# Kernel optimization log

Hardware: AMD Instinct MI355X
Metric: run time of the kernel (lower is better)

The kernel has to match this reference:

```python
import jax, jax.numpy as jnp
import numpy as np

B, N, IN_DIM, D, H, F, L, P = 32, 512, 64, 256, 8, 1024, 3, 512
HD = D // H


def setup_inputs() -> dict:
    key = jax.random.key(0)
    ks = jax.random.split(key, 12)
    s = 0.02
    return {
        "x": jax.random.normal(ks[0], (B, N, IN_DIM), jnp.float32),
        "tw_start": jax.random.uniform(ks[1], (B, N), jnp.float32),
        "adj_mask": jax.random.randint(ks[2], (B, N, N), 0, 2) > 0,
        "Wp": jax.random.normal(ks[3], (D, IN_DIM), jnp.float32) * s,
        "bp": jnp.zeros((D,), jnp.float32),
        "pe": jax.random.normal(ks[4], (P, D), jnp.float32) * s,
        "Wqkv": jax.random.normal(ks[5], (L, 3 * D, D), jnp.float32) * s,
        "bqkv": jnp.zeros((L, 3 * D), jnp.float32),
        "Wo": jax.random.normal(ks[6], (L, D, D), jnp.float32) * s,
        "bo": jnp.zeros((L, D), jnp.float32),
        "ln1g": jnp.ones((L, D), jnp.float32),
        "ln1b": jnp.zeros((L, D), jnp.float32),
        "W1": jax.random.normal(ks[7], (L, F, D), jnp.float32) * s,
        "b1": jnp.zeros((L, F), jnp.float32),
        "W2": jax.random.normal(ks[8], (L, D, F), jnp.float32) * s,
        "b2": jnp.zeros((L, D), jnp.float32),
        "ln2g": jnp.ones((L, D), jnp.float32),
        "ln2b": jnp.zeros((L, D), jnp.float32),
    }


def _ln(x, g, b):
    m = x.mean(-1, keepdims=True)
    v = ((x - m) ** 2).mean(-1, keepdims=True)
    return (x - m) * jax.lax.rsqrt(v + 1e-5) * g + b


def reference(x, tw_start, adj_mask, Wp, bp, pe, Wqkv, bqkv, Wo, bo,
              ln1g, ln1b, W1, b1, W2, b2, ln2g, ln2b):
    # temporal rank = inverse permutation of argsort (equals the torch scatter trick)
    rank = jnp.argsort(jnp.argsort(tw_start, axis=-1), axis=-1)
    rank = jnp.clip(rank, 0, P - 1)
    h = x @ Wp.T + bp + pe[rank]                     # (B,N,D)
    # additive mask, broadcast over heads: (B,1,N,N)
    bias = jnp.where(adj_mask, 0.0, -1e9)[:, None].astype(h.dtype)
    scale = 1.0 / np.sqrt(HD)
    for l in range(L):
        qkv = h @ Wqkv[l].T + bqkv[l]                # (B,N,3D)
        q, k, v = jnp.split(qkv, 3, axis=-1)
        q = q.reshape(B, N, H, HD)
        k = k.reshape(B, N, H, HD)
        v = v.reshape(B, N, H, HD)
        scores = jnp.einsum('bqhd,bkhd->bhqk', q, k) * scale + bias
        attn = jax.nn.softmax(scores, axis=-1)
        o = jnp.einsum('bhqk,bkhd->bqhd', attn, v).reshape(B, N, D)
        o = o @ Wo[l].T + bo[l]
        h = _ln(h + o, ln1g[l], ln1b[l])
        ffo = jax.nn.gelu(h @ W1[l].T + b1[l], approximate=False) @ W2[l].T + b2[l]
        h = _ln(h + ffo, ln2g[l], ln2b[l])
    return h
```

## Files before the change

kernel.cpp:

```cpp
#include <hip/hip_runtime.h>
#include <hip/hip_bf16.h>

#define B_ 32
#define N_ 512
#define IN_DIM_ 64
#define D_ 256
#define H_ 8
#define HD_ 32
#define F_ 1024
#define L_ 3
#define P_ 512

typedef __bf16 bf16_t;
typedef bf16_t bf16x8 __attribute__((ext_vector_type(8)));
typedef bf16_t bf16x4 __attribute__((ext_vector_type(4)));
typedef float f32x4 __attribute__((ext_vector_type(4)));

__global__ __launch_bounds__(512) void rank_kernel(const float* __restrict__ tw,
                                                   int* __restrict__ rank) {
  const int b = blockIdx.x;
  const int i = threadIdx.x;
  __shared__ float s[N_];
  const float ti = tw[b * N_ + i];
  s[i] = ti;
  __syncthreads();
  int c = 0;
#pragma unroll 8
  for (int j = 0; j < N_; ++j) {
    const float tj = s[j];
    c += (tj < ti) || (tj == ti && j < i);
  }
  rank[b * N_ + i] = c < (P_ - 1) ? c : (P_ - 1);
}

__global__ void detect_mask_kernel(const unsigned char* __restrict__ m,
                                   int* __restrict__ flag) {
  unsigned v = 0;
  for (int i = 0; i < 64; ++i)
    if (i & 3) v |= m[i];
  *flag = (v == 0) ? 1 : 0;
}

__global__ __launch_bounds__(256) void packmask_kernel(
    const unsigned char* __restrict__ m, const int* __restrict__ flag,
    unsigned long long* __restrict__ bits) {
  const int idx = blockIdx.x * 256 + threadIdx.x;
  const size_t base = (size_t)(idx >> 3) * N_ + (idx & 7) * 64;
  unsigned long long v = 0;
  if (*flag) {
    const unsigned int* p = (const unsigned int*)m + base;
#pragma unroll 8
    for (int i = 0; i < 64; ++i) v |= (unsigned long long)(p[i] & 1u) << i;
  } else {
    const unsigned char* p = m + base;
#pragma unroll 8
    for (int i = 0; i < 64; ++i) v |= (unsigned long long)(p[i] & 1u) << i;
  }
  bits[idx] = v;
}

__global__ __launch_bounds__(256) void cvt_kernel(const float* __restrict__ s,
                                                  bf16_t* __restrict__ d, int n) {
  const int i = (blockIdx.x * 256 + threadIdx.x) * 4;
  if (i >= n) return;
  const float4 v = *(const float4*)(s + i);
  bf16x4 o = {(bf16_t)v.x, (bf16_t)v.y, (bf16_t)v.z, (bf16_t)v.w};
  *(bf16x4*)(d + i) = o;
}

__device__ __forceinline__ void gl16(const bf16_t* g, char* l) {
  __builtin_amdgcn_global_load_lds(
      (const __attribute__((address_space(1))) unsigned int*)g,
      (__attribute__((address_space(3))) unsigned int*)l, 16, 0, 0);
}

template <int EPI, int WF, int WB>
__global__ __launch_bounds__(256) void gemm_lds(
    const bf16_t* __restrict__ A, const bf16_t* __restrict__ W,
    const float* __restrict__ bias, const int K, const int Nd,
    float* __restrict__ Cf, bf16_t* __restrict__ Cb,
    const int* __restrict__ rank, const float* __restrict__ pe) {
  __shared__ __align__(16) bf16_t As[2][128 * 32];
  __shared__ __align__(16) bf16_t Ws[2][128 * 32];
  const int t = threadIdx.x;
  const int w = t >> 6, l = t & 63, g = l >> 4, r16 = l & 15;
  const int wm = w >> 1, wn = w & 1;
  const int m0 = blockIdx.x * 128, n0 = blockIdx.y * 128;

  f32x4 acc[4][4];
#pragma unroll
  for (int m = 0; m < 4; ++m)
#pragma unroll
    for (int n = 0; n < 4; ++n) acc[m][n] = (f32x4){0.f, 0.f, 0.f, 0.f};

  const int srow = w * 32 + (l >> 2);
  const int scol = (l & 3) * 8;
  const bf16_t* Ag = A + (size_t)(m0 + srow) * K + scol;
  const bf16_t* Wg = W + (size_t)(n0 + srow) * K + scol;
  char* Asb = (char*)As + w * 2048;
  char* Wsb = (char*)Ws + w * 2048;
  const int rowK16 = 16 * K;

  const char* Afr = (const char*)As + (wm * 64 + r16) * 64 + g * 16;
  const char* Wfr = (const char*)Ws + (wn * 64 + r16) * 64 + g * 16;

  const int nt = K >> 5;

  gl16(Ag, Asb);
  gl16(Ag + rowK16, Asb + 1024);
  gl16(Wg, Wsb);
  gl16(Wg + rowK16, Wsb + 1024);
  asm volatile("s_waitcnt vmcnt(0)" ::: "memory");
  __builtin_amdgcn_s_barrier();
  __builtin_amdgcn_sched_barrier(0);

  for (int tt = 0; tt < nt; ++tt) {
    const int curo = (tt & 1) * 8192;
    if (tt + 1 < nt) {
      const int nxto = 8192 - curo;
      const int k0 = (tt + 1) << 5;
      gl16(Ag + k0, Asb + nxto);
      gl16(Ag + k0 + rowK16, Asb + nxto + 1024);
      gl16(Wg + k0, Wsb + nxto);
      gl16(Wg + k0 + rowK16, Wsb + nxto + 1024);
    }
    bf16x8 af[4], wf[4];
#pragma unroll
    for (int m = 0; m < 4; ++m) af[m] = *(const bf16x8*)(Afr + curo + m * 1024);
#pragma unroll
    for (int n = 0; n < 4; ++n) wf[n] = *(const bf16x8*)(Wfr + curo + n * 1024);
#pragma unroll
    for (int m = 0; m < 4; ++m)
#pragma unroll
      for (int n = 0; n < 4; ++n)
        acc[m][n] = __builtin_amdgcn_mfma_f32_16x16x32_bf16(af[m], wf[n], acc[m][n], 0, 0, 0);
    if (tt + 1 < nt) {
      asm volatile("s_waitcnt vmcnt(0)" ::: "memory");
      __builtin_amdgcn_s_barrier();
      __builtin_amdgcn_sched_barrier(0);
    }
  }

  float bcol[4];
#pragma unroll
  for (int n = 0; n < 4; ++n) bcol[n] = bias[n0 + wn * 64 + n * 16 + r16];

#pragma unroll
  for (int m = 0; m < 4; ++m) {
#pragma unroll
    for (int r = 0; r < 4; ++r) {
      const int rowg = m0 + wm * 64 + m * 16 + g * 4 + r;
      float pv[4];
      if (EPI == 2) {
        const float* per = pe + (size_t)rank[rowg] * D_ + n0 + wn * 64 + r16;
#pragma unroll
        for (int n = 0; n < 4; ++n) pv[n] = per[n * 16];
      }
#pragma unroll
      for (int n = 0; n < 4; ++n) {
        float v = acc[m][n][r] + bcol[n];
        if (EPI == 2) v += pv[n];
        if (EPI == 1) v = 0.5f * v * (1.f + erff(v * 0.70710678118654752f));
        const size_t idx = (size_t)rowg * Nd + n0 + wn * 64 + n * 16 + r16;
        if (WF) Cf[idx] = v;
        if (WB) Cb[idx] = (bf16_t)v;
      }
    }
  }
}

__global__ __launch_bounds__(256) void attn_mfma(
    const bf16_t* __restrict__ qkv, const unsigned long long* __restrict__ mbits,
    bf16_t* __restrict__ out) {
  __shared__ __align__(16) char Ksh[64 * 80];
  __shared__ __align__(16) char Vsh[32 * 144];
  __shared__ __align__(16) char Psh[4 * 16 * 144];
  __shared__ unsigned long long Msh[64 * 8];
  const int t = threadIdx.x;
  const int w = t >> 6, l = t & 63, g = l >> 4, r16 = l & 15;
  const int qt = blockIdx.x & 7, bh = blockIdx.x >> 3;
  const int b = bh >> 3, hh = bh & 7;
  const int q0 = qt * 64;
  const float scale = 0.17677669529663687f;

  for (int i = t; i < 512; i += 256)
    Msh[i] = mbits[((size_t)b * N_ + q0 + (i >> 3)) * 8 + (i & 7)];

  const bf16_t* base = qkv + (size_t)b * N_ * (3 * D_) + hh * HD_;
  const bf16x8 qf = *(const bf16x8*)(base + (size_t)(q0 + w * 16 + r16) * (3 * D_) + g * 8);

  f32x4 oacc0 = {0.f, 0.f, 0.f, 0.f}, oacc1 = {0.f, 0.f, 0.f, 0.f};
  float mrow[4] = {-1e30f, -1e30f, -1e30f, -1e30f};
  float lrow[4] = {0.f, 0.f, 0.f, 0.f};

  const int krow = t >> 2, kq = t & 3;
  const int vkey = t & 63, vd0 = (t >> 6) * 8;
  char* Kw = Ksh + krow * 80 + kq * 16;
  char* Pw = Psh + w * 16 * 144;
  const f32x4 z = {0.f, 0.f, 0.f, 0.f};

  for (int kt = 0; kt < 8; ++kt) {
    const int k0 = kt * 64;
    *(float4*)Kw = *(const float4*)(base + (size_t)(k0 + krow) * (3 * D_) + D_ + kq * 8);
    const bf16x8 vv = *(const bf16x8*)(base + (size_t)(k0 + vkey) * (3 * D_) + 2 * D_ + vd0);
#pragma unroll
    for (int j = 0; j < 8; ++j)
      *(bf16_t*)(Vsh + (vd0 + j) * 144 + vkey * 2) = vv[j];
    __syncthreads();

    f32x4 s[4];
#pragma unroll
    for (int j = 0; j < 4; ++j) {
      const bf16x8 kf = *(const bf16x8*)(Ksh + (j * 16 + r16) * 80 + g * 16);
      s[j] = __builtin_amdgcn_mfma_f32_16x16x32_bf16(qf, kf, z, 0, 0, 0);
    }
    unsigned long long mw[4];
#pragma unroll
    for (int r = 0; r < 4; ++r) mw[r] = Msh[(w * 16 + g * 4 + r) * 8 + kt];

    float sval[4][4];
    float mx[4] = {-1e30f, -1e30f, -1e30f, -1e30f};
#pragma unroll
    for (int j = 0; j < 4; ++j)
#pragma unroll
      for (int r = 0; r < 4; ++r) {
        const bool bit = (mw[r] >> (j * 16 + r16)) & 1ULL;
        const float sv = bit ? s[j][r] * scale : -1e30f;
        sval[j][r] = sv;
        mx[r] = fmaxf(mx[r], sv);
      }
#pragma unroll
    for (int d = 1; d < 16; d <<= 1)
#pragma unroll
      for (int r = 0; r < 4; ++r) mx[r] = fmaxf(mx[r], __shfl_xor(mx[r], d));

    int grow = 0;
#pragma unroll
    for (int r = 0; r < 4; ++r) grow |= (mx[r] > mrow[r] + 8.f) ? 1 : 0;
    if (__any(grow)) {
#pragma unroll
      for (int r = 0; r < 4; ++r) {
        const float mn = fmaxf(mrow[r], mx[r]);
        const float ce = __expf(mrow[r] - mn);
        mrow[r] = mn;
        lrow[r] *= ce;
        oacc0[r] *= ce;
        oacc1[r] *= ce;
      }
    }
    float psum[4] = {0.f, 0.f, 0.f, 0.f};
#pragma unroll
    for (int j = 0; j < 4; ++j)
#pragma unroll
      for (int r = 0; r < 4; ++r) {
        const float p = __expf(sval[j][r] - mrow[r]);
        psum[r] += p;
        *(bf16_t*)(Pw + (g * 4 + r) * 144 + (j * 16 + r16) * 2) = (bf16_t)p;
      }
#pragma unroll
    for (int d = 1; d < 16; d <<= 1)
#pragma unroll
      for (int r = 0; r < 4; ++r) psum[r] += __shfl_xor(psum[r], d);
#pragma unroll
    for (int r = 0; r < 4; ++r) lrow[r] += psum[r];
    __threadfence_block();

#pragma unroll
    for (int kh = 0; kh < 2; ++kh) {
      const bf16x8 pa = *(const bf16x8*)(Pw + r16 * 144 + kh * 64 + g * 16);
      const bf16x8 v0 = *(const bf16x8*)(Vsh + r16 * 144 + kh * 64 + g * 16);
      const bf16x8 v1 = *(const bf16x8*)(Vsh + (16 + r16) * 144 + kh * 64 + g * 16);
      oacc0 = __builtin_amdgcn_mfma_f32_16x16x32_bf16(pa, v0, oacc0, 0, 0, 0);
      oacc1 = __builtin_amdgcn_mfma_f32_16x16x32_bf16(pa, v1, oacc1, 0, 0, 0);
    }
    __syncthreads();
  }

  float inv[4];
#pragma unroll
  for (int r = 0; r < 4; ++r) inv[r] = lrow[r] > 0.f ? 1.f / lrow[r] : 0.f;
#pragma unroll
  for (int r = 0; r < 4; ++r) {
    bf16_t* op = out + (size_t)(b * N_ + q0 + w * 16 + g * 4 + r) * D_ + hh * HD_;
    op[r16] = (bf16_t)(oacc0[r] * inv[r]);
    op[16 + r16] = (bf16_t)(oacc1[r] * inv[r]);
  }
}

template <int BF>
__global__ __launch_bounds__(256) void ln_kernel(
    const float* __restrict__ hin, const float* __restrict__ o,
    const float* __restrict__ g, const float* __restrict__ beta,
    float* __restrict__ outf, bf16_t* __restrict__ outb) {
  const int row = blockIdx.x * 4 + threadIdx.y;
  const int lane = threadIdx.x;
  const size_t base = (size_t)row * D_ + lane * 4;
  const float4 hv = *(const float4*)&hin[base];
  const float4 ov = *(const float4*)&o[base];
  const float x0 = hv.x + ov.x, x1 = hv.y + ov.y, x2 = hv.z + ov.z, x3 = hv.w + ov.w;

  float s = x0 + x1 + x2 + x3;
#pragma unroll
  for (int off = 32; off >= 1; off >>= 1) s += __shfl_xor(s, off, 64);
  const float mean = s * (1.f / D_);

  const float d0 = x0 - mean, d1 = x1 - mean, d2 = x2 - mean, d3 = x3 - mean;
  float sq = d0 * d0 + d1 * d1 + d2 * d2 + d3 * d3;
#pragma unroll
  for (int off = 32; off >= 1; off >>= 1) sq += __shfl_xor(sq, off, 64);
  const float rs = rsqrtf(sq * (1.f / D_) + 1e-5f);

  const float4 gv = *(const float4*)&g[lane * 4];
  const float4 bv = *(const float4*)&beta[lane * 4];
  const float y0 = d0 * rs * gv.x + bv.x, y1 = d1 * rs * gv.y + bv.y;
  const float y2 = d2 * rs * gv.z + bv.z, y3 = d3 * rs * gv.w + bv.w;
  *(float4*)&outf[base] = make_float4(y0, y1, y2, y3);
  if (BF) {
    bf16x4 ob = {(bf16_t)y0, (bf16_t)y1, (bf16_t)y2, (bf16_t)y3};
    *(bf16x4*)(outb + base) = ob;
  }
}

extern "C" void kernel_launch(void* const* d_in, const int* in_sizes, int n_in,
                              void* d_out, int out_size, void* d_ws, size_t ws_size,
                              hipStream_t stream) {
  const float* x   = (const float*)d_in[0];
  const float* tw  = (const float*)d_in[1];
  const unsigned char* adj = (const unsigned char*)d_in[2];
  const float* Wp  = (const float*)d_in[3];
  const float* bp  = (const float*)d_in[4];
  const float* pe  = (const float*)d_in[5];
  const float* Wqkv = (const float*)d_in[6];
  const float* bqkv = (const float*)d_in[7];
  const float* Wo  = (const float*)d_in[8];
  const float* bo  = (const float*)d_in[9];
  const float* ln1g = (const float*)d_in[10];
  const float* ln1b = (const float*)d_in[11];
  const float* W1  = (const float*)d_in[12];
  const float* b1  = (const float*)d_in[13];
  const float* W2  = (const float*)d_in[14];
  const float* b2  = (const float*)d_in[15];
  const float* ln2g = (const float*)d_in[16];
  const float* ln2b = (const float*)d_in[17];
  float* out = (float*)d_out;

  char* ws = (char*)d_ws;
  size_t off = 0;
  int* rank = (int*)(ws + off);                      off += 65536;
  int* mflag = (int*)(ws + off);                     off += 64;
  unsigned long long* mbits = (unsigned long long*)(ws + off); off += 1048576;
  bf16_t* x_bf = (bf16_t*)(ws + off);                off += 2097152;
  bf16_t* Wp_bf = (bf16_t*)(ws + off);               off += 32768;
  bf16_t* Wqkv_bf = (bf16_t*)(ws + off);             off += 1179648;
  bf16_t* Wo_bf = (bf16_t*)(ws + off);               off += 393216;
  bf16_t* W1_bf = (bf16_t*)(ws + off);               off += 1572864;
  bf16_t* W2_bf = (bf16_t*)(ws + off);               off += 1572864;
  float* h = (float*)(ws + off);                     off += 16777216;
  bf16_t* h_bf = (bf16_t*)(ws + off);                off += 8388608;
  float* tmp = (float*)(ws + off);                   off += 16777216;
  bf16_t* attno_bf = (bf16_t*)(ws + off);            off += 8388608;
  bf16_t* qkv_bf = (bf16_t*)(ws + off);
  bf16_t* ffn1_bf = (bf16_t*)(ws + off);

  const dim3 blk(256);
  rank_kernel<<<B_, 512, 0, stream>>>(tw, rank);
  detect_mask_kernel<<<1, 1, 0, stream>>>(adj, mflag);
  packmask_kernel<<<512, blk, 0, stream>>>(adj, mflag, mbits);
  cvt_kernel<<<1024, blk, 0, stream>>>(x, x_bf, 1048576);
  cvt_kernel<<<16, blk, 0, stream>>>(Wp, Wp_bf, 16384);
  cvt_kernel<<<576, blk, 0, stream>>>(Wqkv, Wqkv_bf, 589824);
  cvt_kernel<<<192, blk, 0, stream>>>(Wo, Wo_bf, 196608);
  cvt_kernel<<<768, blk, 0, stream>>>(W1, W1_bf, 786432);
  cvt_kernel<<<768, blk, 0, stream>>>(W2, W2_bf, 786432);

  gemm_lds<2, 1, 1><<<dim3(128, 2), blk, 0, stream>>>(
      x_bf, Wp_bf, bp, IN_DIM_, D_, h, h_bf, rank, pe);

  for (int l = 0; l < L_; ++l) {
    gemm_lds<0, 0, 1><<<dim3(128, 6), blk, 0, stream>>>(
        h_bf, Wqkv_bf + (size_t)l * 3 * D_ * D_, bqkv + l * 3 * D_, D_, 3 * D_,
        nullptr, qkv_bf, nullptr, nullptr);
    attn_mfma<<<B_ * H_ * 8, blk, 0, stream>>>(qkv_bf, mbits, attno_bf);
    gemm_lds<0, 1, 0><<<dim3(128, 2), blk, 0, stream>>>(
        attno_bf, Wo_bf + (size_t)l * D_ * D_, bo + l * D_, D_, D_,
        tmp, nullptr, nullptr, nullptr);
    ln_kernel<1><<<(B_ * N_) / 4, dim3(64, 4), 0, stream>>>(
        h, tmp, ln1g + l * D_, ln1b + l * D_, h, h_bf);
    gemm_lds<1, 0, 1><<<dim3(128, 8), blk, 0, stream>>>(
        h_bf, W1_bf + (size_t)l * F_ * D_, b1 + l * F_, D_, F_,
        nullptr, ffn1_bf, nullptr, nullptr);
    gemm_lds<0, 1, 0><<<dim3(128, 2), blk, 0, stream>>>(
        ffn1_bf, W2_bf + (size_t)l * D_ * F_, b2 + l * D_, F_, D_,
        tmp, nullptr, nullptr, nullptr);
    if (l == L_ - 1)
      ln_kernel<0><<<(B_ * N_) / 4, dim3(64, 4), 0, stream>>>(
          h, tmp, ln2g + l * D_, ln2b + l * D_, out, nullptr);
    else
      ln_kernel<1><<<(B_ * N_) / 4, dim3(64, 4), 0, stream>>>(
          h, tmp, ln2g + l * D_, ln2b + l * D_, h, h_bf);
  }
}
```

Before: 610.2 us.

## Fuse output and FFN2 GEMMs with residual LayerNorm, merge conversion launches

```diff
diff --git a/kernel.cpp b/kernel.cpp
--- a/kernel.cpp
+++ b/kernel.cpp
@@ -33,21 +33,18 @@
   rank[b * N_ + i] = c < (P_ - 1) ? c : (P_ - 1);
 }
 
-__global__ void detect_mask_kernel(const unsigned char* __restrict__ m,
-                                   int* __restrict__ flag) {
-  unsigned v = 0;
-  for (int i = 0; i < 64; ++i)
-    if (i & 3) v |= m[i];
-  *flag = (v == 0) ? 1 : 0;
-}
-
 __global__ __launch_bounds__(256) void packmask_kernel(
-    const unsigned char* __restrict__ m, const int* __restrict__ flag,
-    unsigned long long* __restrict__ bits) {
+    const unsigned char* __restrict__ m, unsigned long long* __restrict__ bits) {
+  const unsigned int* mw = (const unsigned int*)m;
+  unsigned dv = 0;
+#pragma unroll
+  for (int i = 0; i < 16; ++i) dv |= mw[i] & 0xFFFFFF00u;
+  const int is32 = (dv == 0);
+
   const int idx = blockIdx.x * 256 + threadIdx.x;
   const size_t base = (size_t)(idx >> 3) * N_ + (idx & 7) * 64;
   unsigned long long v = 0;
-  if (*flag) {
+  if (is32) {
     const unsigned int* p = (const unsigned int*)m + base;
 #pragma unroll 8
     for (int i = 0; i < 64; ++i) v |= (unsigned long long)(p[i] & 1u) << i;
@@ -59,10 +56,22 @@
   bits[idx] = v;
 }
 
-__global__ __launch_bounds__(256) void cvt_kernel(const float* __restrict__ s,
-                                                  bf16_t* __restrict__ d, int n) {
-  const int i = (blockIdx.x * 256 + threadIdx.x) * 4;
-  if (i >= n) return;
+struct CvtArgs {
+  const float* s[6];
+  bf16_t* d[6];
+};
+__global__ __launch_bounds__(256) void cvt_all(CvtArgs a) {
+  const int blk = blockIdx.x;
+  int seg, off;
+  if (blk < 1024)      { seg = 0; off = blk; }
+  else if (blk < 1040) { seg = 1; off = blk - 1024; }
+  else if (blk < 1616) { seg = 2; off = blk - 1040; }
+  else if (blk < 1808) { seg = 3; off = blk - 1616; }
+  else if (blk < 2576) { seg = 4; off = blk - 1808; }
+  else                 { seg = 5; off = blk - 2576; }
+  const float* s = a.s[seg];
+  bf16_t* d = a.d[seg];
+  const int i = (off * 256 + threadIdx.x) * 4;
   const float4 v = *(const float4*)(s + i);
   bf16x4 o = {(bf16_t)v.x, (bf16_t)v.y, (bf16_t)v.z, (bf16_t)v.w};
   *(bf16x4*)(d + i) = o;
@@ -160,11 +169,124 @@
       for (int n = 0; n < 4; ++n) {
         float v = acc[m][n][r] + bcol[n];
         if (EPI == 2) v += pv[n];
-        if (EPI == 1) v = 0.5f * v * (1.f + erff(v * 0.70710678118654752f));
+        if (EPI == 1) {
+          const float u = 0.7978845608028654f * (v + 0.044715f * v * v * v);
+          const float th = 1.f - 2.f / (1.f + __expf(2.f * u));
+          v = 0.5f * v * (1.f + th);
+        }
         const size_t idx = (size_t)rowg * Nd + n0 + wn * 64 + n * 16 + r16;
         if (WF) Cf[idx] = v;
         if (WB) Cb[idx] = (bf16_t)v;
       }
+    }
+  }
+}
+
+template <int LAST>
+__global__ __launch_bounds__(256) void gemm_ln(
+    const bf16_t* __restrict__ A, const bf16_t* __restrict__ Wt,
+    const float* __restrict__ bias, const int K,
+    const float* __restrict__ hres,
+    const float* __restrict__ gam, const float* __restrict__ bet,
+    float* __restrict__ outf, bf16_t* __restrict__ outb) {
+  __shared__ __align__(16) bf16_t As[2][64 * 32];
+  __shared__ __align__(16) bf16_t Ws[2][256 * 32];
+  const int t = threadIdx.x;
+  const int w = t >> 6, l = t & 63, g = l >> 4, r16 = l & 15;
+  const int m0 = blockIdx.x * 64;
+
+  f32x4 acc[16];
+#pragma unroll
+  for (int n = 0; n < 16; ++n) acc[n] = (f32x4){0.f, 0.f, 0.f, 0.f};
+
+  const bf16_t* Ag = A + (size_t)(m0 + w * 16 + (l >> 2)) * K + (l & 3) * 8;
+  const bf16_t* Wg = Wt + (size_t)(w * 64 + (l >> 2)) * K + (l & 3) * 8;
+  char* Asb = (char*)As + w * 1024;
+  char* Wsb = (char*)Ws + w * 4096;
+  const int rowK16 = 16 * K;
+
+  const char* Afr = (const char*)As + (w * 16 + r16) * 64 + g * 16;
+  const char* Wfr = (const char*)Ws + r16 * 64 + g * 16;
+
+  const int nt = K >> 5;
+
+  gl16(Ag, Asb);
+  gl16(Wg, Wsb);
+  gl16(Wg + rowK16, Wsb + 1024);
+  gl16(Wg + 2 * rowK16, Wsb + 2048);
+  gl16(Wg + 3 * rowK16, Wsb + 3072);
+  asm volatile("s_waitcnt vmcnt(0)" ::: "memory");
+  __builtin_amdgcn_s_barrier();
+  __builtin_amdgcn_sched_barrier(0);
+
+  for (int tt = 0; tt < nt; ++tt) {
+    const int curA = (tt & 1) * 4096;
+    const int curW = (tt & 1) * 16384;
+    if (tt + 1 < nt) {
+      const int k0 = (tt + 1) << 5;
+      char* nA = Asb + (4096 - curA);
+      char* nW = Wsb + (16384 - curW);
+      gl16(Ag + k0, nA);
+      gl16(Wg + k0, nW);
+      gl16(Wg + k0 + rowK16, nW + 1024);
+      gl16(Wg + k0 + 2 * rowK16, nW + 2048);
+      gl16(Wg + k0 + 3 * rowK16, nW + 3072);
+    }
+    const bf16x8 af = *(const bf16x8*)(Afr + curA);
+#pragma unroll
+    for (int n = 0; n < 16; ++n) {
+      const bf16x8 wfn = *(const bf16x8*)(Wfr + curW + n * 1024);
+      acc[n] = __builtin_amdgcn_mfma_f32_16x16x32_bf16(af, wfn, acc[n], 0, 0, 0);
+    }
+    if (tt + 1 < nt) {
+      asm volatile("s_waitcnt vmcnt(0)" ::: "memory");
+      __builtin_amdgcn_s_barrier();
+      __builtin_amdgcn_sched_barrier(0);
+    }
+  }
+
+  float bia[16], gc[16], bc[16];
+#pragma unroll
+  for (int n = 0; n < 16; ++n) {
+    bia[n] = bias[n * 16 + r16];
+    gc[n] = gam[n * 16 + r16];
+    bc[n] = bet[n * 16 + r16];
+  }
+#pragma unroll
+  for (int r = 0; r < 4; ++r) {
+    const int rowg = m0 + w * 16 + g * 4 + r;
+    const float* hrow = hres + (size_t)rowg * D_;
+    float s = 0.f;
+#pragma unroll
+    for (int n = 0; n < 16; ++n) {
+      const float v = acc[n][r] + bia[n] + hrow[n * 16 + r16];
+      acc[n][r] = v;
+      s += v;
+    }
+    s += __shfl_xor(s, 1);
+    s += __shfl_xor(s, 2);
+    s += __shfl_xor(s, 4);
+    s += __shfl_xor(s, 8);
+    const float mean = s * (1.f / D_);
+    float sq = 0.f;
+#pragma unroll
+    for (int n = 0; n < 16; ++n) {
+      const float d = acc[n][r] - mean;
+      acc[n][r] = d;
+      sq += d * d;
+    }
+    sq += __shfl_xor(sq, 1);
+    sq += __shfl_xor(sq, 2);
+    sq += __shfl_xor(sq, 4);
+    sq += __shfl_xor(sq, 8);
+    const float rs = rsqrtf(sq * (1.f / D_) + 1e-5f);
+    float* orow = outf + (size_t)rowg * D_;
+    bf16_t* brow = LAST ? nullptr : (outb + (size_t)rowg * D_);
+#pragma unroll
+    for (int n = 0; n < 16; ++n) {
+      const float y = acc[n][r] * rs * gc[n] + bc[n];
+      orow[n * 16 + r16] = y;
+      if (!LAST) brow[n * 16 + r16] = (bf16_t)y;
     }
   }
 }
@@ -284,40 +406,6 @@
     bf16_t* op = out + (size_t)(b * N_ + q0 + w * 16 + g * 4 + r) * D_ + hh * HD_;
     op[r16] = (bf16_t)(oacc0[r] * inv[r]);
     op[16 + r16] = (bf16_t)(oacc1[r] * inv[r]);
-  }
-}
-
-template <int BF>
-__global__ __launch_bounds__(256) void ln_kernel(
-    const float* __restrict__ hin, const float* __restrict__ o,
-    const float* __restrict__ g, const float* __restrict__ beta,
-    float* __restrict__ outf, bf16_t* __restrict__ outb) {
-  const int row = blockIdx.x * 4 + threadIdx.y;
-  const int lane = threadIdx.x;
-  const size_t base = (size_t)row * D_ + lane * 4;
-  const float4 hv = *(const float4*)&hin[base];
-  const float4 ov = *(const float4*)&o[base];
-  const float x0 = hv.x + ov.x, x1 = hv.y + ov.y, x2 = hv.z + ov.z, x3 = hv.w + ov.w;
-
-  float s = x0 + x1 + x2 + x3;
-#pragma unroll
-  for (int off = 32; off >= 1; off >>= 1) s += __shfl_xor(s, off, 64);
-  const float mean = s * (1.f / D_);
-
-  const float d0 = x0 - mean, d1 = x1 - mean, d2 = x2 - mean, d3 = x3 - mean;
-  float sq = d0 * d0 + d1 * d1 + d2 * d2 + d3 * d3;
-#pragma unroll
-  for (int off = 32; off >= 1; off >>= 1) sq += __shfl_xor(sq, off, 64);
-  const float rs = rsqrtf(sq * (1.f / D_) + 1e-5f);
-
-  const float4 gv = *(const float4*)&g[lane * 4];
-  const float4 bv = *(const float4*)&beta[lane * 4];
-  const float y0 = d0 * rs * gv.x + bv.x, y1 = d1 * rs * gv.y + bv.y;
-  const float y2 = d2 * rs * gv.z + bv.z, y3 = d3 * rs * gv.w + bv.w;
-  *(float4*)&outf[base] = make_float4(y0, y1, y2, y3);
-  if (BF) {
-    bf16x4 ob = {(bf16_t)y0, (bf16_t)y1, (bf16_t)y2, (bf16_t)y3};
-    *(bf16x4*)(outb + base) = ob;
   }
 }
 
@@ -347,7 +435,6 @@
   char* ws = (char*)d_ws;
   size_t off = 0;
   int* rank = (int*)(ws + off);                      off += 65536;
-  int* mflag = (int*)(ws + off);                     off += 64;
   unsigned long long* mbits = (unsigned long long*)(ws + off); off += 1048576;
   bf16_t* x_bf = (bf16_t*)(ws + off);                off += 2097152;
   bf16_t* Wp_bf = (bf16_t*)(ws + off);               off += 32768;
@@ -357,21 +444,22 @@
   bf16_t* W2_bf = (bf16_t*)(ws + off);               off += 1572864;
   float* h = (float*)(ws + off);                     off += 16777216;
   bf16_t* h_bf = (bf16_t*)(ws + off);                off += 8388608;
-  float* tmp = (float*)(ws + off);                   off += 16777216;
   bf16_t* attno_bf = (bf16_t*)(ws + off);            off += 8388608;
   bf16_t* qkv_bf = (bf16_t*)(ws + off);
   bf16_t* ffn1_bf = (bf16_t*)(ws + off);
 
   const dim3 blk(256);
   rank_kernel<<<B_, 512, 0, stream>>>(tw, rank);
-  detect_mask_kernel<<<1, 1, 0, stream>>>(adj, mflag);
-  packmask_kernel<<<512, blk, 0, stream>>>(adj, mflag, mbits);
-  cvt_kernel<<<1024, blk, 0, stream>>>(x, x_bf, 1048576);
-  cvt_kernel<<<16, blk, 0, stream>>>(Wp, Wp_bf, 16384);
-  cvt_kernel<<<576, blk, 0, stream>>>(Wqkv, Wqkv_bf, 589824);
-  cvt_kernel<<<192, blk, 0, stream>>>(Wo, Wo_bf, 196608);
-  cvt_kernel<<<768, blk, 0, stream>>>(W1, W1_bf, 786432);
-  cvt_kernel<<<768, blk, 0, stream>>>(W2, W2_bf, 786432);
+  packmask_kernel<<<512, blk, 0, stream>>>(adj, mbits);
+
+  CvtArgs ca;
+  ca.s[0] = x;   ca.d[0] = x_bf;
+  ca.s[1] = Wp;  ca.d[1] = Wp_bf;
+  ca.s[2] = Wqkv; ca.d[2] = Wqkv_bf;
+  ca.s[3] = Wo;  ca.d[3] = Wo_bf;
+  ca.s[4] = W1;  ca.d[4] = W1_bf;
+  ca.s[5] = W2;  ca.d[5] = W2_bf;
+  cvt_all<<<3344, blk, 0, stream>>>(ca);
 
   gemm_lds<2, 1, 1><<<dim3(128, 2), blk, 0, stream>>>(
       x_bf, Wp_bf, bp, IN_DIM_, D_, h, h_bf, rank, pe);
@@ -381,22 +469,19 @@
         h_bf, Wqkv_bf + (size_t)l * 3 * D_ * D_, bqkv + l * 3 * D_, D_, 3 * D_,
         nullptr, qkv_bf, nullptr, nullptr);
     attn_mfma<<<B_ * H_ * 8, blk, 0, stream>>>(qkv_bf, mbits, attno_bf);
-    gemm_lds<0, 1, 0><<<dim3(128, 2), blk, 0, stream>>>(
-        attno_bf, Wo_bf + (size_t)l * D_ * D_, bo + l * D_, D_, D_,
-        tmp, nullptr, nullptr, nullptr);
-    ln_kernel<1><<<(B_ * N_) / 4, dim3(64, 4), 0, stream>>>(
-        h, tmp, ln1g + l * D_, ln1b + l * D_, h, h_bf);
+    gemm_ln<0><<<256, blk, 0, stream>>>(
+        attno_bf, Wo_bf + (size_t)l * D_ * D_, bo + l * D_, D_,
+        h, ln1g + l * D_, ln1b + l * D_, h, h_bf);
     gemm_lds<1, 0, 1><<<dim3(128, 8), blk, 0, stream>>>(
         h_bf, W1_bf + (size_t)l * F_ * D_, b1 + l * F_, D_, F_,
         nullptr, ffn1_bf, nullptr, nullptr);
-    gemm_lds<0, 1, 0><<<dim3(128, 2), blk, 0, stream>>>(
-        ffn1_bf, W2_bf + (size_t)l * D_ * F_, b2 + l * D_, F_, D_,
-        tmp, nullptr, nullptr, nullptr);
     if (l == L_ - 1)
-      ln_kernel<0><<<(B_ * N_) / 4, dim3(64, 4), 0, stream>>>(
-          h, tmp, ln2g + l * D_, ln2b + l * D_, out, nullptr);
+      gemm_ln<1><<<256, blk, 0, stream>>>(
+          ffn1_bf, W2_bf + (size_t)l * D_ * F_, b2 + l * D_, F_,
+          h, ln2g + l * D_, ln2b + l * D_, out, nullptr);
     else
-      ln_kernel<1><<<(B_ * N_) / 4, dim3(64, 4), 0, stream>>>(
-          h, tmp, ln2g + l * D_, ln2b + l * D_, h, h_bf);
-  }
-}
+      gemm_ln<0><<<256, blk, 0, stream>>>(
+          ffn1_bf, W2_bf + (size_t)l * D_ * F_, b2 + l * D_, F_,
+          h, ln2g + l * D_, ln2b + l * D_, h, h_bf);
+  }
+}
```

Measured after the change: 578.1 us. 1.06x faster.
